# Performance work log

Hardware: AMD Instinct MI355X
Metric: run time of the kernel (lower is better)

The kernel has to match this reference:

```python
import jax, jax.numpy as jnp
import numpy as np

N, E = 50000, 800000
D_IN, D_HID, D_OUT = 128, 256, 128


def setup_inputs() -> dict:
    key = jax.random.key(0)
    k = jax.random.split(key, 7)
    x = jax.random.normal(k[0], (N, D_IN), dtype=jnp.float32)
    edge_src = jax.random.randint(k[1], (E,), 0, N, dtype=jnp.int32)
    edge_dst = jax.random.randint(k[2], (E,), 0, N, dtype=jnp.int32)
    s1 = 1.0 / np.sqrt(2 * D_IN)
    s2 = 1.0 / np.sqrt(2 * D_HID)
    W1 = jax.random.uniform(k[3], (2 * D_IN, D_HID), jnp.float32, -s1, s1)
    b1 = jax.random.uniform(k[4], (D_HID,), jnp.float32, -s1, s1)
    W2 = jax.random.uniform(k[5], (2 * D_HID, D_OUT), jnp.float32, -s2, s2)
    b2 = jax.random.uniform(k[6], (D_OUT,), jnp.float32, -s2, s2)
    return {"x": x, "edge_src": edge_src, "edge_dst": edge_dst,
            "W1": W1, "b1": b1, "W2": W2, "b2": b2}


def _sage_layer(h, edge_src, edge_dst, W, b, inv_deg):
    # mean-pool neighbor features: gather [E, D] then segment-sum to [N, D]
    msgs = h[edge_src]
    agg = jax.ops.segment_sum(msgs, edge_dst, num_segments=h.shape[0]) * inv_deg
    y = jnp.concatenate([h, agg], axis=1)  # [N, 2D]
    return y @ W + b


def reference(x, edge_src, edge_dst, W1, b1, W2, b2):
    n = x.shape[0]
    deg = jax.ops.segment_sum(jnp.ones_like(edge_dst, dtype=x.dtype), edge_dst,
                              num_segments=n)
    inv_deg = (1.0 / jnp.maximum(deg, 1.0))[:, None]  # isolated nodes -> zeros
    h = _sage_layer(x, edge_src, edge_dst, W1, b1, inv_deg)
    h = jax.nn.relu(h)
    # dropout is identity in eval mode
    h = _sage_layer(h, edge_src, edge_dst, W2, b2, inv_deg)
    return jax.nn.log_softmax(h, axis=1)
```

## Files before the change

### kernel.cpp

```cpp
#include <hip/hip_runtime.h>
#include <cstdint>
#include <cstddef>

typedef __attribute__((ext_vector_type(8))) short bf16x8;
typedef __attribute__((ext_vector_type(4))) float f32x4;
typedef __attribute__((ext_vector_type(2))) float f32x2;

__device__ inline short bf16_rne(float f) {
  unsigned u = __builtin_bit_cast(unsigned, f);
  u += 0x7fff + ((u >> 16) & 1);
  return (short)(u >> 16);
}

__device__ inline float bf16lo(unsigned v) { return __builtin_bit_cast(float, v << 16); }
__device__ inline float bf16hi(unsigned v) { return __builtin_bit_cast(float, v & 0xffff0000u); }

__device__ inline unsigned pack2(float a, float b) {
  return ((unsigned)(unsigned short)bf16_rne(a)) | (((unsigned)(unsigned short)bf16_rne(b)) << 16);
}


__global__ __launch_bounds__(256) void prep_scatter_kernel(
    const float* __restrict__ W1, const float* __restrict__ W2, const float* __restrict__ b2,
    const float* __restrict__ x, short* __restrict__ B1p, short* __restrict__ B2p,
    float* __restrict__ bias2, unsigned* __restrict__ A1u, unsigned* __restrict__ xf8,
    int nquads, const int* __restrict__ esrc, const int* __restrict__ edst, int E, int EPB,
    int* __restrict__ counters, int NB, int SB, int SLACK, unsigned* __restrict__ bedge) {
  __shared__ int h[512];
  __shared__ int base[512];
  int b = blockIdx.x;
  int tid = threadIdx.x;
  if (b < SB) {
    for (int t = tid; t < NB; t += 256) h[t] = 0;
    __syncthreads();
    int start = b * EPB, end = min(E, start + EPB);
    for (int i = start + tid; i < end; i += 256) atomicAdd(&h[((unsigned)edst[i]) >> 7], 1);
    __syncthreads();
    for (int t = tid; t < NB; t += 256) {
      int c = h[t];
      base[t] = (c > 0) ? atomicAdd(&counters[t], c) : 0;
      h[t] = 0;
    }
    __syncthreads();
    for (int i = start + tid; i < end; i += 256) {
      unsigned d = (unsigned)edst[i];
      unsigned bk = d >> 7;
      int p = base[bk] + atomicAdd(&h[bk], 1);
      bedge[(size_t)bk * SLACK + p] = ((d & 127u) << 24) | (unsigned)esrc[i];
    }
    return;
  }
  int b2i = b - SB;
  if (b2i < 512) {
    int mode = b2i >> 8;
    int idx = (b2i & 255) * 256 + tid;
    int j = idx & 7;
    int L = (idx >> 3) & 63;
    int nt = (idx >> 9) & 15;
    int kb = idx >> 13;
    int k = kb * 32 + (L >> 4) * 8 + j;
    int n = nt * 16 + (L & 15);
    if (mode == 0) {
      B1p[idx] = bf16_rne(W1[(size_t)k * 256 + n]);
    } else {
      float v = (n < 128) ? W2[(size_t)k * 128 + n] : W2[(size_t)(256 + k) * 128 + (n - 128)];
      B2p[idx] = bf16_rne(v);
    }
  } else if (b2i == 512) {
    bias2[tid] = (tid < 128) ? b2[tid] : 0.0f;
  } else {
    int idx = (b2i - 513) * 256 + tid;
    if (idx < nquads) {
      int n = idx >> 5, q = idx & 31;
      float4 v = ((const float4*)x)[idx];
      ((uint2*)A1u)[(size_t)n * 64 + q] = make_uint2(pack2(v.x, v.y), pack2(v.z, v.w));
      int pk = __builtin_amdgcn_cvt_pk_fp8_f32(v.x, v.y, 0, false);
      pk = __builtin_amdgcn_cvt_pk_fp8_f32(v.z, v.w, pk, true);
      xf8[(size_t)n * 32 + q] = (unsigned)pk;
    } else if (idx < nquads + 32) {
      int n = idx >> 5, q = idx & 31;
      ((uint2*)A1u)[(size_t)n * 64 + q] = make_uint2(0u, 0u);
      xf8[(size_t)n * 32 + q] = 0u;
    }
  }
}

__global__ __launch_bounds__(256) void build_csr(const unsigned* __restrict__ bedge,
                                                 const int* __restrict__ counters,
                                                 int NB, int SLACK, int N,
                                                 int* __restrict__ offsets,
                                                 int* __restrict__ oend,
                                                 float* __restrict__ inv_deg,
                                                 int* __restrict__ ssrc) {
  __shared__ int buf[128];
  __shared__ int cur[128];
  __shared__ int lim[128];
  int b = blockIdx.x, tid = threadIdx.x;
  int cntE = counters[b];
  int rb = b * SLACK;
  if (tid < 128) buf[tid] = 0;
  __syncthreads();
  for (int i = tid; i < cntE; i += 256) atomicAdd(&buf[bedge[(size_t)rb + i] >> 24], 1);
  __syncthreads();
  int cnt = (tid < 128) ? buf[tid] : 0;
  int pcnt = min((cnt + 3) & ~3, 64);
  if (tid < 128) buf[tid] = pcnt;
  __syncthreads();
  #pragma unroll
  for (int off = 1; off < 128; off <<= 1) {
    int t = (tid >= off && tid < 128) ? buf[tid - off] : 0;
    __syncthreads();
    if (tid < 128) buf[tid] += t;
    __syncthreads();
  }
  int excl = 0;
  if (tid < 128) {
    excl = buf[tid] - pcnt;
    int node = (b << 7) + tid;
    if (node < N) {
      offsets[node] = rb + excl;
      oend[node]    = rb + excl + pcnt;
      inv_deg[node] = 1.0f / fmaxf((float)cnt, 1.0f);
    }
  }
  __syncthreads();
  if (tid < 128) {
    cur[tid] = rb + excl;
    lim[tid] = rb + excl + pcnt;
  }
  __syncthreads();
  for (int i = tid; i < cntE; i += 256) {
    unsigned e2 = bedge[(size_t)rb + i];
    int nd = e2 >> 24;
    int p = atomicAdd(&cur[nd], 1);
    if (p < lim[nd]) ssrc[p] = (int)(e2 & 0xFFFFFFu);
  }
  __syncthreads();
  if (tid < 128) {
    int base0 = rb + excl;
    for (int p2 = cnt; p2 < pcnt; ++p2) ssrc[base0 + p2] = N;
  }
}

#define CVT8(U, A0, A1, A2, A3, A4, A5, A6, A7)                                        \
  {                                                                                    \
    f32x2 p_, q_;                                                                      \
    p_ = __builtin_amdgcn_cvt_pk_f32_fp8((U).x, false);                                \
    q_ = __builtin_amdgcn_cvt_pk_f32_fp8((U).x, true);                                 \
    A0 += p_[0]; A1 += p_[1]; A2 += q_[0]; A3 += q_[1];                                \
    p_ = __builtin_amdgcn_cvt_pk_f32_fp8((U).y, false);                                \
    q_ = __builtin_amdgcn_cvt_pk_f32_fp8((U).y, true);                                 \
    A4 += p_[0]; A5 += p_[1]; A6 += q_[0]; A7 += q_[1];                                \
  }

__global__ __launch_bounds__(256) void agg1_kernel(const uint2* __restrict__ X8,
                                                   const int* __restrict__ offsets,
                                                   const int* __restrict__ oend,
                                                   const int* __restrict__ ssrc,
                                                   const float* __restrict__ inv_deg,
                                                   uint4* __restrict__ A1q, int N) {
  int node = blockIdx.x * 4 + (threadIdx.x >> 6);
  if (node >= N) return;
  int lane = threadIdx.x & 63;
  int g = lane >> 4;
  int l = lane & 15;
  int s = offsets[node];
  int nq = (oend[node] - s) >> 2;
  int sv = ssrc[s + lane];
  float a0=0.f,a1=0.f,a2=0.f,a3=0.f,a4=0.f,a5=0.f,a6=0.f,a7=0.f;
  int q = 0;
  for (; q + 4 <= nq; q += 4) {
    int sA = __shfl(sv, (q + 0) * 4 + g, 64);
    int sB = __shfl(sv, (q + 1) * 4 + g, 64);
    int sC = __shfl(sv, (q + 2) * 4 + g, 64);
    int sD = __shfl(sv, (q + 3) * 4 + g, 64);
    uint2 u = X8[((size_t)(unsigned)sA << 4) + l];
    uint2 v = X8[((size_t)(unsigned)sB << 4) + l];
    uint2 w = X8[((size_t)(unsigned)sC << 4) + l];
    uint2 z = X8[((size_t)(unsigned)sD << 4) + l];
    CVT8(u, a0,a1,a2,a3,a4,a5,a6,a7);
    CVT8(v, a0,a1,a2,a3,a4,a5,a6,a7);
    CVT8(w, a0,a1,a2,a3,a4,a5,a6,a7);
    CVT8(z, a0,a1,a2,a3,a4,a5,a6,a7);
  }
  for (; q < nq; ++q) {
    int sA = __shfl(sv, q * 4 + g, 64);
    uint2 u = X8[((size_t)(unsigned)sA << 4) + l];
    CVT8(u, a0,a1,a2,a3,a4,a5,a6,a7);
  }
  a0 += __shfl_xor(a0,16,64); a0 += __shfl_xor(a0,32,64);
  a1 += __shfl_xor(a1,16,64); a1 += __shfl_xor(a1,32,64);
  a2 += __shfl_xor(a2,16,64); a2 += __shfl_xor(a2,32,64);
  a3 += __shfl_xor(a3,16,64); a3 += __shfl_xor(a3,32,64);
  a4 += __shfl_xor(a4,16,64); a4 += __shfl_xor(a4,32,64);
  a5 += __shfl_xor(a5,16,64); a5 += __shfl_xor(a5,32,64);
  a6 += __shfl_xor(a6,16,64); a6 += __shfl_xor(a6,32,64);
  a7 += __shfl_xor(a7,16,64); a7 += __shfl_xor(a7,32,64);
  if (g == 0) {
    float id = inv_deg[node];
    A1q[((size_t)node << 5) + 16 + l] =
        make_uint4(pack2(a0 * id, a1 * id), pack2(a2 * id, a3 * id),
                   pack2(a4 * id, a5 * id), pack2(a6 * id, a7 * id));
  }
}

__global__ __launch_bounds__(512, 2) void gemm_fused(const short* __restrict__ A,
                                                     const short* __restrict__ B1,
                                                     const short* __restrict__ B2,
                                                     const float* __restrict__ bias1,
                                                     const float* __restrict__ bias2,
                                                     short* __restrict__ utop,
                                                     unsigned char* __restrict__ t2,
                                                     int S, int Nvalid) {
  __shared__ char hls[2 * 16 * 512];
  int tid = threadIdx.x;
  int wv = tid >> 6;
  int lane = tid & 63;
  int role = wv >> 2;
  int w = wv & 3;
  int rowf = lane & 15;
  int g = lane >> 4;

  const short* Bp = role ? B2 : B1;
  const float* bias = role ? bias2 : bias1;

  bf16x8 breg[8][4];
  #pragma unroll
  for (int kb = 0; kb < 8; ++kb)
    #pragma unroll
    for (int j = 0; j < 4; ++j)
      breg[kb][j] = *(const bf16x8*)(Bp + ((size_t)((kb * 16 + w * 4 + j) * 64 + lane)) * 8);

  f32x4 bj[4];
  #pragma unroll
  for (int j = 0; j < 4; ++j)
    bj[j] = *(const f32x4*)(bias + w * 64 + j * 16 + g * 4);

  for (int i = 0;; ++i) {
    int sP = blockIdx.x + i * gridDim.x;
    int sC = blockIdx.x + (i - 1) * gridDim.x;
    bool anyP = sP < S;
    bool anyC = (i > 0) && (sC < S);
    if (!anyP && !anyC) break;

    if (role == 0) {
      if (anyP) {
        int row0 = sP * 16;
        const short* Arow = A + (size_t)(row0 + rowf) * 256 + g * 8;
        bf16x8 afr[8];
        #pragma unroll
        for (int kb = 0; kb < 8; ++kb) afr[kb] = *(const bf16x8*)(Arow + kb * 32);
        f32x4 acc[4];
        #pragma unroll
        for (int j = 0; j < 4; ++j) acc[j] = (f32x4)(0.0f);
        __builtin_amdgcn_s_setprio(1);
        #pragma unroll
        for (int kb = 0; kb < 8; ++kb)
          #pragma unroll
          for (int j = 0; j < 4; ++j)
            acc[j] = __builtin_amdgcn_mfma_f32_16x16x32_bf16(breg[kb][j], afr[kb], acc[j], 0, 0, 0);
        __builtin_amdgcn_s_setprio(0);
        int buf = (i & 1) * 8192;
        #pragma unroll
        for (int j = 0; j < 4; ++j) {
          float v0 = fmaxf(acc[j][0] + bj[j][0], 0.0f);
          float v1 = fmaxf(acc[j][1] + bj[j][1], 0.0f);
          float v2 = fmaxf(acc[j][2] + bj[j][2], 0.0f);
          float v3 = fmaxf(acc[j][3] + bj[j][3], 0.0f);
          int c0 = w * 64 + j * 16 + g * 4;
          int chunk = c0 >> 3;
          int swz = chunk ^ rowf ^ ((chunk & 1) << 4);
          *(uint2*)(hls + buf + rowf * 512 + swz * 16 + ((c0 & 4) << 1)) =
              make_uint2(pack2(v0, v1), pack2(v2, v3));
        }
      }
    } else {
      if (anyC) {
        int buf = ((i - 1) & 1) * 8192;
        bf16x8 afr[8];
        #pragma unroll
        for (int kb = 0; kb < 8; ++kb) {
          int chunk = kb * 4 + g;
          int swz = chunk ^ rowf ^ ((chunk & 1) << 4);
          afr[kb] = *(const bf16x8*)(hls + buf + rowf * 512 + swz * 16);
        }
        f32x4 acc[4];
        #pragma unroll
        for (int j = 0; j < 4; ++j) acc[j] = (f32x4)(0.0f);
        __builtin_amdgcn_s_setprio(1);
        #pragma unroll
        for (int kb = 0; kb < 8; ++kb)
          #pragma unroll
          for (int j = 0; j < 4; ++j)
            acc[j] = __builtin_amdgcn_mfma_f32_16x16x32_bf16(breg[kb][j], afr[kb], acc[j], 0, 0, 0);
        __builtin_amdgcn_s_setprio(0);
        int row = sC * 16 + rowf;
        bool live = row < Nvalid;
        #pragma unroll
        for (int j = 0; j < 4; ++j) {
          float v0 = live ? acc[j][0] + bj[j][0] : 0.0f;
          float v1 = live ? acc[j][1] + bj[j][1] : 0.0f;
          float v2 = live ? acc[j][2] + bj[j][2] : 0.0f;
          float v3 = live ? acc[j][3] + bj[j][3] : 0.0f;
          int c0 = w * 64 + j * 16 + g * 4;
          if (w < 2) {
            *(uint2*)(utop + (size_t)row * 128 + c0) = make_uint2(pack2(v0, v1), pack2(v2, v3));
          } else {
            int pk = __builtin_amdgcn_cvt_pk_fp8_f32(v0, v1, 0, false);
            pk = __builtin_amdgcn_cvt_pk_fp8_f32(v2, v3, pk, true);
            *(unsigned*)(t2 + (size_t)row * 128 + (c0 - 128)) = (unsigned)pk;
          }
        }
      }
    }
    __syncthreads();
  }
}

__global__ __launch_bounds__(256) void final_kernel(const uint4* __restrict__ utopq,
                                                    const uint2* __restrict__ T2,
                                                    const int* __restrict__ offsets,
                                                    const int* __restrict__ oend,
                                                    const int* __restrict__ ssrc,
                                                    const float* __restrict__ inv_deg,
                                                    float4* __restrict__ out4, int N) {
  int node = blockIdx.x * 4 + (threadIdx.x >> 6);
  if (node >= N) return;
  int lane = threadIdx.x & 63;
  int g = lane >> 4;
  int l = lane & 15;
  int s = offsets[node];
  int nq = (oend[node] - s) >> 2;
  int sv = ssrc[s + lane];
  float a0=0.f,a1=0.f,a2=0.f,a3=0.f,a4=0.f,a5=0.f,a6=0.f,a7=0.f;
  int q = 0;
  for (; q + 4 <= nq; q += 4) {
    int sA = __shfl(sv, (q + 0) * 4 + g, 64);
    int sB = __shfl(sv, (q + 1) * 4 + g, 64);
    int sC = __shfl(sv, (q + 2) * 4 + g, 64);
    int sD = __shfl(sv, (q + 3) * 4 + g, 64);
    uint2 u = T2[((size_t)(unsigned)sA << 4) + l];
    uint2 v = T2[((size_t)(unsigned)sB << 4) + l];
    uint2 w = T2[((size_t)(unsigned)sC << 4) + l];
    uint2 z = T2[((size_t)(unsigned)sD << 4) + l];
    CVT8(u, a0,a1,a2,a3,a4,a5,a6,a7);
    CVT8(v, a0,a1,a2,a3,a4,a5,a6,a7);
    CVT8(w, a0,a1,a2,a3,a4,a5,a6,a7);
    CVT8(z, a0,a1,a2,a3,a4,a5,a6,a7);
  }
  for (; q < nq; ++q) {
    int sA = __shfl(sv, q * 4 + g, 64);
    uint2 u = T2[((size_t)(unsigned)sA << 4) + l];
    CVT8(u, a0,a1,a2,a3,a4,a5,a6,a7);
  }
  a0 += __shfl_xor(a0,16,64); a0 += __shfl_xor(a0,32,64);
  a1 += __shfl_xor(a1,16,64); a1 += __shfl_xor(a1,32,64);
  a2 += __shfl_xor(a2,16,64); a2 += __shfl_xor(a2,32,64);
  a3 += __shfl_xor(a3,16,64); a3 += __shfl_xor(a3,32,64);
  a4 += __shfl_xor(a4,16,64); a4 += __shfl_xor(a4,32,64);
  a5 += __shfl_xor(a5,16,64); a5 += __shfl_xor(a5,32,64);
  a6 += __shfl_xor(a6,16,64); a6 += __shfl_xor(a6,32,64);
  a7 += __shfl_xor(a7,16,64); a7 += __shfl_xor(a7,32,64);
  if (g == 0) {
    float id = inv_deg[node];
    uint4 U = utopq[((size_t)node << 4) + l];
    float v0 = bf16lo(U.x) + a0 * id;
    float v1 = bf16hi(U.x) + a1 * id;
    float v2 = bf16lo(U.y) + a2 * id;
    float v3 = bf16hi(U.y) + a3 * id;
    float v4 = bf16lo(U.z) + a4 * id;
    float v5 = bf16hi(U.z) + a5 * id;
    float v6 = bf16lo(U.w) + a6 * id;
    float v7 = bf16hi(U.w) + a7 * id;
    float m = fmaxf(fmaxf(fmaxf(v0, v1), fmaxf(v2, v3)), fmaxf(fmaxf(v4, v5), fmaxf(v6, v7)));
    #pragma unroll
    for (int off = 1; off < 16; off <<= 1) m = fmaxf(m, __shfl_xor(m, off, 16));
    float su = expf(v0 - m) + expf(v1 - m) + expf(v2 - m) + expf(v3 - m) +
               expf(v4 - m) + expf(v5 - m) + expf(v6 - m) + expf(v7 - m);
    #pragma unroll
    for (int off = 1; off < 16; off <<= 1) su += __shfl_xor(su, off, 16);
    float ls = m + logf(su);
    out4[((size_t)node << 5) + l * 2]     = make_float4(v0 - ls, v1 - ls, v2 - ls, v3 - ls);
    out4[((size_t)node << 5) + l * 2 + 1] = make_float4(v4 - ls, v5 - ls, v6 - ls, v7 - ls);
  }
}

extern "C" void kernel_launch(void* const* d_in, const int* in_sizes, int n_in,
                              void* d_out, int out_size, void* d_ws, size_t ws_size,
                              hipStream_t stream) {
  const float* x        = (const float*)d_in[0];
  const int*   edge_src = (const int*)d_in[1];
  const int*   edge_dst = (const int*)d_in[2];
  const float* W1       = (const float*)d_in[3];
  const float* b1       = (const float*)d_in[4];
  const float* W2       = (const float*)d_in[5];
  const float* b2       = (const float*)d_in[6];
  float* out = (float*)d_out;

  const int D_IN = 128;
  const int N = in_sizes[0] / D_IN;
  const int E = in_sizes[1];
  const int M_pad = ((N + 128) / 128) * 128;

  const int SB = 512;
  const int EPB = (E + SB - 1) / SB;
  const int NB = (N + 127) >> 7;
  const int SLACK = 3072;

  char* ws = (char*)d_ws;
  size_t p = 0;
  auto take = [&](size_t bytes) -> size_t {
    size_t r = p;
    p += (bytes + 255) & ~(size_t)255;
    return r;
  };
  size_t cnt_off   = take((size_t)NB * 4);
  size_t bedge_off = take((size_t)NB * SLACK * 4);
  size_t offs_off  = take((size_t)N * 4);
  size_t oend_off  = take((size_t)N * 4);
  size_t inv_off   = take((size_t)N * 4);
  size_t ssrc_off  = take((size_t)NB * SLACK * 4 + 256);
  size_t A1_off    = take((size_t)M_pad * 256 * 2);
  size_t xf8_off   = take((size_t)M_pad * 128);
  size_t B1p_off   = take((size_t)256 * 256 * 2);
  size_t B2p_off   = take((size_t)256 * 256 * 2);
  size_t bias2_off = take((size_t)256 * 4);
  size_t utop_off  = take((size_t)M_pad * 128 * 2);
  size_t t2_off    = take((size_t)M_pad * 128);
  (void)ws_size;

  int*   counters = (int*)(ws + cnt_off);
  unsigned* bedge = (unsigned*)(ws + bedge_off);
  int*   offsets  = (int*)(ws + offs_off);
  int*   oendp    = (int*)(ws + oend_off);
  float* inv_deg  = (float*)(ws + inv_off);
  int*   ssrc     = (int*)(ws + ssrc_off);
  unsigned* A1u   = (unsigned*)(ws + A1_off);
  unsigned* xf8   = (unsigned*)(ws + xf8_off);
  short* B1p      = (short*)(ws + B1p_off);
  short* B2p      = (short*)(ws + B2p_off);
  float* bias2    = (float*)(ws + bias2_off);
  short* utop     = (short*)(ws + utop_off);
  unsigned char* t2f8 = (unsigned char*)(ws + t2_off);

  hipMemsetAsync(counters, 0, (size_t)NB * 4, stream);
  {
    int nquads = N * 32;
    int nqb = (nquads + 32 + 255) / 256;
    int grid = SB + 513 + nqb;
    prep_scatter_kernel<<<grid, 256, 0, stream>>>(W1, W2, b2, x, B1p, B2p, bias2, A1u, xf8,
                                                  nquads, edge_src, edge_dst, E, EPB,
                                                  counters, NB, SB, SLACK, bedge);
  }
  build_csr<<<NB, 256, 0, stream>>>(bedge, counters, NB, SLACK, N, offsets, oendp, inv_deg, ssrc);

  agg1_kernel<<<(N + 3) / 4, 256, 0, stream>>>((const uint2*)xf8, offsets, oendp, ssrc, inv_deg,
                                               (uint4*)A1u, N);
  {
    int S = M_pad / 16;
    gemm_fused<<<256, 512, 0, stream>>>((const short*)A1u, B1p, B2p, b1, bias2, utop, t2f8, S, N);
  }
  final_kernel<<<(N + 3) / 4, 256, 0, stream>>>((const uint4*)utop, (const uint2*)t2f8,
                                                offsets, oendp, ssrc, inv_deg, (float4*)out, N);
}
```

Baseline: 195.7 us.

## Fuse CSR build into aggregation kernels using per-bucket LDS neighbor lists

```diff
diff --git a/kernel.cpp b/kernel.cpp
--- a/kernel.cpp
+++ b/kernel.cpp
@@ -85,63 +85,6 @@
   }
 }
 
-__global__ __launch_bounds__(256) void build_csr(const unsigned* __restrict__ bedge,
-                                                 const int* __restrict__ counters,
-                                                 int NB, int SLACK, int N,
-                                                 int* __restrict__ offsets,
-                                                 int* __restrict__ oend,
-                                                 float* __restrict__ inv_deg,
-                                                 int* __restrict__ ssrc) {
-  __shared__ int buf[128];
-  __shared__ int cur[128];
-  __shared__ int lim[128];
-  int b = blockIdx.x, tid = threadIdx.x;
-  int cntE = counters[b];
-  int rb = b * SLACK;
-  if (tid < 128) buf[tid] = 0;
-  __syncthreads();
-  for (int i = tid; i < cntE; i += 256) atomicAdd(&buf[bedge[(size_t)rb + i] >> 24], 1);
-  __syncthreads();
-  int cnt = (tid < 128) ? buf[tid] : 0;
-  int pcnt = min((cnt + 3) & ~3, 64);
-  if (tid < 128) buf[tid] = pcnt;
-  __syncthreads();
-  #pragma unroll
-  for (int off = 1; off < 128; off <<= 1) {
-    int t = (tid >= off && tid < 128) ? buf[tid - off] : 0;
-    __syncthreads();
-    if (tid < 128) buf[tid] += t;
-    __syncthreads();
-  }
-  int excl = 0;
-  if (tid < 128) {
-    excl = buf[tid] - pcnt;
-    int node = (b << 7) + tid;
-    if (node < N) {
-      offsets[node] = rb + excl;
-      oend[node]    = rb + excl + pcnt;
-      inv_deg[node] = 1.0f / fmaxf((float)cnt, 1.0f);
-    }
-  }
-  __syncthreads();
-  if (tid < 128) {
-    cur[tid] = rb + excl;
-    lim[tid] = rb + excl + pcnt;
-  }
-  __syncthreads();
-  for (int i = tid; i < cntE; i += 256) {
-    unsigned e2 = bedge[(size_t)rb + i];
-    int nd = e2 >> 24;
-    int p = atomicAdd(&cur[nd], 1);
-    if (p < lim[nd]) ssrc[p] = (int)(e2 & 0xFFFFFFu);
-  }
-  __syncthreads();
-  if (tid < 128) {
-    int base0 = rb + excl;
-    for (int p2 = cnt; p2 < pcnt; ++p2) ssrc[base0 + p2] = N;
-  }
-}
-
 #define CVT8(U, A0, A1, A2, A3, A4, A5, A6, A7)                                        \
   {                                                                                    \
     f32x2 p_, q_;                                                                      \
@@ -153,54 +96,104 @@
     A4 += p_[0]; A5 += p_[1]; A6 += q_[0]; A7 += q_[1];                                \
   }
 
-__global__ __launch_bounds__(256) void agg1_kernel(const uint2* __restrict__ X8,
-                                                   const int* __restrict__ offsets,
-                                                   const int* __restrict__ oend,
-                                                   const int* __restrict__ ssrc,
-                                                   const float* __restrict__ inv_deg,
-                                                   uint4* __restrict__ A1q, int N) {
-  int node = blockIdx.x * 4 + (threadIdx.x >> 6);
-  if (node >= N) return;
-  int lane = threadIdx.x & 63;
+#define LDS_CAP 8256
+
+#define BUILD_BUCKET_LISTS(bedge, counters, SLACK, N)                                  \
+  int cntE = counters[bkt];                                                            \
+  size_t rb = (size_t)bkt * SLACK;                                                     \
+  if (tid < 128) cnt[tid] = 0;                                                         \
+  __syncthreads();                                                                     \
+  for (int i = tid; i < cntE; i += 512) atomicAdd(&cnt[bedge[rb + i] >> 24], 1);       \
+  __syncthreads();                                                                     \
+  {                                                                                    \
+    int c_ = (tid < 128) ? cnt[tid] : 0;                                               \
+    int pcnt_ = min((c_ + 3) & ~3, 64);                                                \
+    if (tid < 128) sbuf[tid] = pcnt_;                                                  \
+    __syncthreads();                                                                   \
+    _Pragma("unroll")                                                                  \
+    for (int o = 1; o < 128; o <<= 1) {                                                \
+      int t_ = (tid >= o && tid < 128) ? sbuf[tid - o] : 0;                            \
+      __syncthreads();                                                                 \
+      if (tid < 128) sbuf[tid] += t_;                                                  \
+      __syncthreads();                                                                 \
+    }                                                                                  \
+    if (tid < 128) {                                                                   \
+      int excl_ = sbuf[tid] - pcnt_;                                                   \
+      off[tid] = excl_;                                                                \
+      cur[tid] = excl_;                                                                \
+      lim[tid] = excl_ + pcnt_;                                                        \
+    }                                                                                  \
+  }                                                                                    \
+  __syncthreads();                                                                     \
+  for (int i = tid; i < cntE; i += 512) {                                              \
+    unsigned e2 = bedge[rb + i];                                                       \
+    int nd = e2 >> 24;                                                                 \
+    int p = atomicAdd(&cur[nd], 1);                                                    \
+    if (p < lim[nd]) lst[p] = (int)(e2 & 0xFFFFFFu);                                   \
+  }                                                                                    \
+  __syncthreads();                                                                     \
+  if (tid < 128) {                                                                     \
+    for (int p = off[tid] + cnt[tid]; p < lim[tid]; ++p) lst[p] = N;                   \
+  }                                                                                    \
+  __syncthreads();
+
+__global__ __launch_bounds__(512) void agg1_bucket(const uint2* __restrict__ X8,
+                                                   const unsigned* __restrict__ bedge,
+                                                   const int* __restrict__ counters,
+                                                   int SLACK, int N, int SPLIT,
+                                                   uint4* __restrict__ A1q) {
+  __shared__ int cnt[128], off[128], lim[128], cur[128], sbuf[128];
+  __shared__ int lst[LDS_CAP];
+  int bkt = blockIdx.x / SPLIT;
+  int sub = blockIdx.x % SPLIT;
+  int tid = threadIdx.x;
+  BUILD_BUCKET_LISTS(bedge, counters, SLACK, N)
+  int wv = tid >> 6;
+  int lane = tid & 63;
   int g = lane >> 4;
   int l = lane & 15;
-  int s = offsets[node];
-  int nq = (oend[node] - s) >> 2;
-  int sv = ssrc[s + lane];
-  float a0=0.f,a1=0.f,a2=0.f,a3=0.f,a4=0.f,a5=0.f,a6=0.f,a7=0.f;
-  int q = 0;
-  for (; q + 4 <= nq; q += 4) {
-    int sA = __shfl(sv, (q + 0) * 4 + g, 64);
-    int sB = __shfl(sv, (q + 1) * 4 + g, 64);
-    int sC = __shfl(sv, (q + 2) * 4 + g, 64);
-    int sD = __shfl(sv, (q + 3) * 4 + g, 64);
-    uint2 u = X8[((size_t)(unsigned)sA << 4) + l];
-    uint2 v = X8[((size_t)(unsigned)sB << 4) + l];
-    uint2 w = X8[((size_t)(unsigned)sC << 4) + l];
-    uint2 z = X8[((size_t)(unsigned)sD << 4) + l];
-    CVT8(u, a0,a1,a2,a3,a4,a5,a6,a7);
-    CVT8(v, a0,a1,a2,a3,a4,a5,a6,a7);
-    CVT8(w, a0,a1,a2,a3,a4,a5,a6,a7);
-    CVT8(z, a0,a1,a2,a3,a4,a5,a6,a7);
-  }
-  for (; q < nq; ++q) {
-    int sA = __shfl(sv, q * 4 + g, 64);
-    uint2 u = X8[((size_t)(unsigned)sA << 4) + l];
-    CVT8(u, a0,a1,a2,a3,a4,a5,a6,a7);
-  }
-  a0 += __shfl_xor(a0,16,64); a0 += __shfl_xor(a0,32,64);
-  a1 += __shfl_xor(a1,16,64); a1 += __shfl_xor(a1,32,64);
-  a2 += __shfl_xor(a2,16,64); a2 += __shfl_xor(a2,32,64);
-  a3 += __shfl_xor(a3,16,64); a3 += __shfl_xor(a3,32,64);
-  a4 += __shfl_xor(a4,16,64); a4 += __shfl_xor(a4,32,64);
-  a5 += __shfl_xor(a5,16,64); a5 += __shfl_xor(a5,32,64);
-  a6 += __shfl_xor(a6,16,64); a6 += __shfl_xor(a6,32,64);
-  a7 += __shfl_xor(a7,16,64); a7 += __shfl_xor(a7,32,64);
-  if (g == 0) {
-    float id = inv_deg[node];
-    A1q[((size_t)node << 5) + 16 + l] =
-        make_uint4(pack2(a0 * id, a1 * id), pack2(a2 * id, a3 * id),
-                   pack2(a4 * id, a5 * id), pack2(a6 * id, a7 * id));
+  for (int t = 0; t < 4; ++t) {
+    int ln = sub * 32 + wv * 4 + t;
+    int node = (bkt << 7) + ln;
+    if (node >= N) continue;
+    int s = off[ln];
+    int nq = (lim[ln] - s) >> 2;
+    int sv = lst[s + lane];
+    float a0=0.f,a1=0.f,a2=0.f,a3=0.f,a4=0.f,a5=0.f,a6=0.f,a7=0.f;
+    int q = 0;
+    for (; q + 4 <= nq; q += 4) {
+      int sA = __shfl(sv, (q + 0) * 4 + g, 64);
+      int sB = __shfl(sv, (q + 1) * 4 + g, 64);
+      int sC = __shfl(sv, (q + 2) * 4 + g, 64);
+      int sD = __shfl(sv, (q + 3) * 4 + g, 64);
+      uint2 u = X8[((size_t)(unsigned)sA << 4) + l];
+      uint2 v = X8[((size_t)(unsigned)sB << 4) + l];
+      uint2 w = X8[((size_t)(unsigned)sC << 4) + l];
+      uint2 z = X8[((size_t)(unsigned)sD << 4) + l];
+      CVT8(u, a0,a1,a2,a3,a4,a5,a6,a7);
+      CVT8(v, a0,a1,a2,a3,a4,a5,a6,a7);
+      CVT8(w, a0,a1,a2,a3,a4,a5,a6,a7);
+      CVT8(z, a0,a1,a2,a3,a4,a5,a6,a7);
+    }
+    for (; q < nq; ++q) {
+      int sA = __shfl(sv, q * 4 + g, 64);
+      uint2 u = X8[((size_t)(unsigned)sA << 4) + l];
+      CVT8(u, a0,a1,a2,a3,a4,a5,a6,a7);
+    }
+    a0 += __shfl_xor(a0,16,64); a0 += __shfl_xor(a0,32,64);
+    a1 += __shfl_xor(a1,16,64); a1 += __shfl_xor(a1,32,64);
+    a2 += __shfl_xor(a2,16,64); a2 += __shfl_xor(a2,32,64);
+    a3 += __shfl_xor(a3,16,64); a3 += __shfl_xor(a3,32,64);
+    a4 += __shfl_xor(a4,16,64); a4 += __shfl_xor(a4,32,64);
+    a5 += __shfl_xor(a5,16,64); a5 += __shfl_xor(a5,32,64);
+    a6 += __shfl_xor(a6,16,64); a6 += __shfl_xor(a6,32,64);
+    a7 += __shfl_xor(a7,16,64); a7 += __shfl_xor(a7,32,64);
+    if (g == 0) {
+      float id = 1.0f / fmaxf((float)cnt[ln], 1.0f);
+      A1q[((size_t)node << 5) + 16 + l] =
+          make_uint4(pack2(a0 * id, a1 * id), pack2(a2 * id, a3 * id),
+                     pack2(a4 * id, a5 * id), pack2(a6 * id, a7 * id));
+    }
   }
 }
 
@@ -317,71 +310,80 @@
   }
 }
 
-__global__ __launch_bounds__(256) void final_kernel(const uint4* __restrict__ utopq,
+__global__ __launch_bounds__(512) void final_bucket(const uint4* __restrict__ utopq,
                                                     const uint2* __restrict__ T2,
-                                                    const int* __restrict__ offsets,
-                                                    const int* __restrict__ oend,
-                                                    const int* __restrict__ ssrc,
-                                                    const float* __restrict__ inv_deg,
-                                                    float4* __restrict__ out4, int N) {
-  int node = blockIdx.x * 4 + (threadIdx.x >> 6);
-  if (node >= N) return;
-  int lane = threadIdx.x & 63;
+                                                    const unsigned* __restrict__ bedge,
+                                                    const int* __restrict__ counters,
+                                                    int SLACK, int N, int SPLIT,
+                                                    float4* __restrict__ out4) {
+  __shared__ int cnt[128], off[128], lim[128], cur[128], sbuf[128];
+  __shared__ int lst[LDS_CAP];
+  int bkt = blockIdx.x / SPLIT;
+  int sub = blockIdx.x % SPLIT;
+  int tid = threadIdx.x;
+  BUILD_BUCKET_LISTS(bedge, counters, SLACK, N)
+  int wv = tid >> 6;
+  int lane = tid & 63;
   int g = lane >> 4;
   int l = lane & 15;
-  int s = offsets[node];
-  int nq = (oend[node] - s) >> 2;
-  int sv = ssrc[s + lane];
-  float a0=0.f,a1=0.f,a2=0.f,a3=0.f,a4=0.f,a5=0.f,a6=0.f,a7=0.f;
-  int q = 0;
-  for (; q + 4 <= nq; q += 4) {
-    int sA = __shfl(sv, (q + 0) * 4 + g, 64);
-    int sB = __shfl(sv, (q + 1) * 4 + g, 64);
-    int sC = __shfl(sv, (q + 2) * 4 + g, 64);
-    int sD = __shfl(sv, (q + 3) * 4 + g, 64);
-    uint2 u = T2[((size_t)(unsigned)sA << 4) + l];
-    uint2 v = T2[((size_t)(unsigned)sB << 4) + l];
-    uint2 w = T2[((size_t)(unsigned)sC << 4) + l];
-    uint2 z = T2[((size_t)(unsigned)sD << 4) + l];
-    CVT8(u, a0,a1,a2,a3,a4,a5,a6,a7);
-    CVT8(v, a0,a1,a2,a3,a4,a5,a6,a7);
-    CVT8(w, a0,a1,a2,a3,a4,a5,a6,a7);
-    CVT8(z, a0,a1,a2,a3,a4,a5,a6,a7);
-  }
-  for (; q < nq; ++q) {
-    int sA = __shfl(sv, q * 4 + g, 64);
-    uint2 u = T2[((size_t)(unsigned)sA << 4) + l];
-    CVT8(u, a0,a1,a2,a3,a4,a5,a6,a7);
-  }
-  a0 += __shfl_xor(a0,16,64); a0 += __shfl_xor(a0,32,64);
-  a1 += __shfl_xor(a1,16,64); a1 += __shfl_xor(a1,32,64);
-  a2 += __shfl_xor(a2,16,64); a2 += __shfl_xor(a2,32,64);
-  a3 += __shfl_xor(a3,16,64); a3 += __shfl_xor(a3,32,64);
-  a4 += __shfl_xor(a4,16,64); a4 += __shfl_xor(a4,32,64);
-  a5 += __shfl_xor(a5,16,64); a5 += __shfl_xor(a5,32,64);
-  a6 += __shfl_xor(a6,16,64); a6 += __shfl_xor(a6,32,64);
-  a7 += __shfl_xor(a7,16,64); a7 += __shfl_xor(a7,32,64);
-  if (g == 0) {
-    float id = inv_deg[node];
-    uint4 U = utopq[((size_t)node << 4) + l];
-    float v0 = bf16lo(U.x) + a0 * id;
-    float v1 = bf16hi(U.x) + a1 * id;
-    float v2 = bf16lo(U.y) + a2 * id;
-    float v3 = bf16hi(U.y) + a3 * id;
-    float v4 = bf16lo(U.z) + a4 * id;
-    float v5 = bf16hi(U.z) + a5 * id;
-    float v6 = bf16lo(U.w) + a6 * id;
-    float v7 = bf16hi(U.w) + a7 * id;
-    float m = fmaxf(fmaxf(fmaxf(v0, v1), fmaxf(v2, v3)), fmaxf(fmaxf(v4, v5), fmaxf(v6, v7)));
-    #pragma unroll
-    for (int off = 1; off < 16; off <<= 1) m = fmaxf(m, __shfl_xor(m, off, 16));
-    float su = expf(v0 - m) + expf(v1 - m) + expf(v2 - m) + expf(v3 - m) +
-               expf(v4 - m) + expf(v5 - m) + expf(v6 - m) + expf(v7 - m);
-    #pragma unroll
-    for (int off = 1; off < 16; off <<= 1) su += __shfl_xor(su, off, 16);
-    float ls = m + logf(su);
-    out4[((size_t)node << 5) + l * 2]     = make_float4(v0 - ls, v1 - ls, v2 - ls, v3 - ls);
-    out4[((size_t)node << 5) + l * 2 + 1] = make_float4(v4 - ls, v5 - ls, v6 - ls, v7 - ls);
+  for (int t = 0; t < 4; ++t) {
+    int ln = sub * 32 + wv * 4 + t;
+    int node = (bkt << 7) + ln;
+    if (node >= N) continue;
+    int s = off[ln];
+    int nq = (lim[ln] - s) >> 2;
+    int sv = lst[s + lane];
+    float a0=0.f,a1=0.f,a2=0.f,a3=0.f,a4=0.f,a5=0.f,a6=0.f,a7=0.f;
+    int q = 0;
+    for (; q + 4 <= nq; q += 4) {
+      int sA = __shfl(sv, (q + 0) * 4 + g, 64);
+      int sB = __shfl(sv, (q + 1) * 4 + g, 64);
+      int sC = __shfl(sv, (q + 2) * 4 + g, 64);
+      int sD = __shfl(sv, (q + 3) * 4 + g, 64);
+      uint2 u = T2[((size_t)(unsigned)sA << 4) + l];
+      uint2 v = T2[((size_t)(unsigned)sB << 4) + l];
+      uint2 w = T2[((size_t)(unsigned)sC << 4) + l];
+      uint2 z = T2[((size_t)(unsigned)sD << 4) + l];
+      CVT8(u, a0,a1,a2,a3,a4,a5,a6,a7);
+      CVT8(v, a0,a1,a2,a3,a4,a5,a6,a7);
+      CVT8(w, a0,a1,a2,a3,a4,a5,a6,a7);
+      CVT8(z, a0,a1,a2,a3,a4,a5,a6,a7);
+    }
+    for (; q < nq; ++q) {
+      int sA = __shfl(sv, q * 4 + g, 64);
+      uint2 u = T2[((size_t)(unsigned)sA << 4) + l];
+      CVT8(u, a0,a1,a2,a3,a4,a5,a6,a7);
+    }
+    a0 += __shfl_xor(a0,16,64); a0 += __shfl_xor(a0,32,64);
+    a1 += __shfl_xor(a1,16,64); a1 += __shfl_xor(a1,32,64);
+    a2 += __shfl_xor(a2,16,64); a2 += __shfl_xor(a2,32,64);
+    a3 += __shfl_xor(a3,16,64); a3 += __shfl_xor(a3,32,64);
+    a4 += __shfl_xor(a4,16,64); a4 += __shfl_xor(a4,32,64);
+    a5 += __shfl_xor(a5,16,64); a5 += __shfl_xor(a5,32,64);
+    a6 += __shfl_xor(a6,16,64); a6 += __shfl_xor(a6,32,64);
+    a7 += __shfl_xor(a7,16,64); a7 += __shfl_xor(a7,32,64);
+    if (g == 0) {
+      float id = 1.0f / fmaxf((float)cnt[ln], 1.0f);
+      uint4 U = utopq[((size_t)node << 4) + l];
+      float v0 = bf16lo(U.x) + a0 * id;
+      float v1 = bf16hi(U.x) + a1 * id;
+      float v2 = bf16lo(U.y) + a2 * id;
+      float v3 = bf16hi(U.y) + a3 * id;
+      float v4 = bf16lo(U.z) + a4 * id;
+      float v5 = bf16hi(U.z) + a5 * id;
+      float v6 = bf16lo(U.w) + a6 * id;
+      float v7 = bf16hi(U.w) + a7 * id;
+      float m = fmaxf(fmaxf(fmaxf(v0, v1), fmaxf(v2, v3)), fmaxf(fmaxf(v4, v5), fmaxf(v6, v7)));
+      #pragma unroll
+      for (int o = 1; o < 16; o <<= 1) m = fmaxf(m, __shfl_xor(m, o, 16));
+      float su = expf(v0 - m) + expf(v1 - m) + expf(v2 - m) + expf(v3 - m) +
+                 expf(v4 - m) + expf(v5 - m) + expf(v6 - m) + expf(v7 - m);
+      #pragma unroll
+      for (int o = 1; o < 16; o <<= 1) su += __shfl_xor(su, o, 16);
+      float ls = m + logf(su);
+      out4[((size_t)node << 5) + l * 2]     = make_float4(v0 - ls, v1 - ls, v2 - ls, v3 - ls);
+      out4[((size_t)node << 5) + l * 2 + 1] = make_float4(v4 - ls, v5 - ls, v6 - ls, v7 - ls);
+    }
   }
 }
 
@@ -406,6 +408,7 @@
   const int EPB = (E + SB - 1) / SB;
   const int NB = (N + 127) >> 7;
   const int SLACK = 3072;
+  const int SPLIT = 4;
 
   char* ws = (char*)d_ws;
   size_t p = 0;
@@ -416,10 +419,6 @@
   };
   size_t cnt_off   = take((size_t)NB * 4);
   size_t bedge_off = take((size_t)NB * SLACK * 4);
-  size_t offs_off  = take((size_t)N * 4);
-  size_t oend_off  = take((size_t)N * 4);
-  size_t inv_off   = take((size_t)N * 4);
-  size_t ssrc_off  = take((size_t)NB * SLACK * 4 + 256);
   size_t A1_off    = take((size_t)M_pad * 256 * 2);
   size_t xf8_off   = take((size_t)M_pad * 128);
   size_t B1p_off   = take((size_t)256 * 256 * 2);
@@ -431,10 +430,6 @@
 
   int*   counters = (int*)(ws + cnt_off);
   unsigned* bedge = (unsigned*)(ws + bedge_off);
-  int*   offsets  = (int*)(ws + offs_off);
-  int*   oendp    = (int*)(ws + oend_off);
-  float* inv_deg  = (float*)(ws + inv_off);
-  int*   ssrc     = (int*)(ws + ssrc_off);
   unsigned* A1u   = (unsigned*)(ws + A1_off);
   unsigned* xf8   = (unsigned*)(ws + xf8_off);
   short* B1p      = (short*)(ws + B1p_off);
@@ -452,14 +447,12 @@
                                                   nquads, edge_src, edge_dst, E, EPB,
                                                   counters, NB, SB, SLACK, bedge);
   }
-  build_csr<<<NB, 256, 0, stream>>>(bedge, counters, NB, SLACK, N, offsets, oendp, inv_deg, ssrc);
-
-  agg1_kernel<<<(N + 3) / 4, 256, 0, stream>>>((const uint2*)xf8, offsets, oendp, ssrc, inv_deg,
-                                               (uint4*)A1u, N);
+  agg1_bucket<<<NB * SPLIT, 512, 0, stream>>>((const uint2*)xf8, bedge, counters,
+                                              SLACK, N, SPLIT, (uint4*)A1u);
   {
     int S = M_pad / 16;
     gemm_fused<<<256, 512, 0, stream>>>((const short*)A1u, B1p, B2p, b1, bias2, utop, t2f8, S, N);
   }
-  final_kernel<<<(N + 3) / 4, 256, 0, stream>>>((const uint4*)utop, (const uint2*)t2f8,
-                                                offsets, oendp, ssrc, inv_deg, (float4*)out, N);
-}
+  final_bucket<<<NB * SPLIT, 512, 0, stream>>>((const uint4*)utop, (const uint2*)t2f8,
+                                               bedge, counters, SLACK, N, SPLIT, (float4*)out);
+}
```

After: 210.5 us. 7.6% more time.
